# Kernel optimization log

Hardware: AMD Instinct MI355X
Metric: run time of the kernel (lower is better)

The kernel has to match this reference:

```python
import jax, jax.numpy as jnp
import numpy as np

N, E = 100000, 1000000
IN_C, OUT_C, EDGE_D = 64, 16, 8


def setup_inputs() -> dict:
    key = jax.random.key(0)
    ks = jax.random.split(key, 11)
    s = 0.1  # param scale
    return {
        "x": jax.random.normal(ks[0], (N, IN_C), jnp.float32),
        "edge_attr": jax.random.normal(ks[1], (E, EDGE_D), jnp.float32),
        "col": jax.random.randint(ks[2], (E,), 0, N, jnp.int32),
        "W_lin": jax.random.normal(ks[3], (IN_C, OUT_C), jnp.float32) * s,
        "b_lin": jax.random.normal(ks[4], (OUT_C,), jnp.float32) * s,
        "W_edge": jax.random.normal(ks[5], (EDGE_D, OUT_C), jnp.float32) * s,
        "b_edge": jax.random.normal(ks[6], (OUT_C,), jnp.float32) * s,
        "w1": jax.random.normal(ks[7], (OUT_C,), jnp.float32) * s,  # Linear(1, C) weight
        "b1": jax.random.normal(ks[8], (OUT_C,), jnp.float32) * s,
        "w2": jax.random.normal(ks[9], (OUT_C,), jnp.float32) * s,  # Linear(C, 1) weight
        "b2": jax.random.normal(ks[10], (1,), jnp.float32) * s,
    }


def reference(x, edge_attr, col, W_lin, b_lin, W_edge, b_edge, w1, b1, w2, b2):
    # node transform: [N, C]
    h = x @ W_lin + b_lin
    # edge attr transform: [E, C]
    ea = edge_attr @ W_edge + b_edge
    # gather source node features per edge: [E, C]
    nv = h[col]
    # [E, 2C]
    combined = jnp.concatenate([nv, ea], axis=-1)
    # per-scalar MLP: Linear(1,C) -> ReLU -> Linear(C,1)
    # hid: [E, 2C, C]; scores: [E, 2C]
    hid = jax.nn.relu(combined[..., None] * w1 + b1)
    scores = hid @ w2 + b2
    # softmax over the 2C axis
    attn = jax.nn.softmax(scores, axis=1)
    # repeat_interleave(2, dim=1): each feature column duplicated -> [E, 2C]
    nv2 = jnp.repeat(nv, 2, axis=1)
    return nv2 * attn
```

## Files before the change

### kernel.cpp

```cpp
#include <hip/hip_runtime.h>
#include <math.h>

#define IN_C 64
#define OUT_C 16

typedef float f4 __attribute__((ext_vector_type(4)));
typedef float f2 __attribute__((ext_vector_type(2)));

__global__ __launch_bounds__(256) void node_linear_kernel(
    const float* __restrict__ x, const float* __restrict__ W_lin,
    const float* __restrict__ b_lin, float* __restrict__ h, int N)
{
    __shared__ float sW[IN_C * OUT_C];
    __shared__ float sb[OUT_C];
    for (int i = threadIdx.x; i < IN_C * OUT_C; i += blockDim.x) sW[i] = W_lin[i];
    if (threadIdx.x < OUT_C) sb[threadIdx.x] = b_lin[threadIdx.x];
    __syncthreads();

    int n = blockIdx.x * blockDim.x + threadIdx.x;
    if (n >= N) return;

    float acc[OUT_C];
    #pragma unroll
    for (int j = 0; j < OUT_C; j++) acc[j] = sb[j];

    const f4* xr = (const f4*)(x + (size_t)n * IN_C);
    #pragma unroll
    for (int k4 = 0; k4 < IN_C / 4; k4++) {
        f4 xv = __builtin_nontemporal_load(xr + k4);
        #pragma unroll
        for (int kk = 0; kk < 4; kk++) {
            const int k = k4 * 4 + kk;
            const float xs = xv[kk];
            const f4* wrow = (const f4*)(sW + k * OUT_C);
            #pragma unroll
            for (int jq = 0; jq < 4; jq++) {
                f4 wv = wrow[jq];
                acc[jq * 4 + 0] = fmaf(xs, wv[0], acc[jq * 4 + 0]);
                acc[jq * 4 + 1] = fmaf(xs, wv[1], acc[jq * 4 + 1]);
                acc[jq * 4 + 2] = fmaf(xs, wv[2], acc[jq * 4 + 2]);
                acc[jq * 4 + 3] = fmaf(xs, wv[3], acc[jq * 4 + 3]);
            }
        }
    }

    f4* hr = (f4*)(h + (size_t)n * OUT_C);
    #pragma unroll
    for (int jq = 0; jq < 4; jq++) {
        f4 o;
        o[0] = acc[jq * 4 + 0]; o[1] = acc[jq * 4 + 1];
        o[2] = acc[jq * 4 + 2]; o[3] = acc[jq * 4 + 3];
        hr[jq] = o;
    }
}

__global__ __launch_bounds__(256) void edge_attn8_kernel(
    const float* __restrict__ edge_attr, const int* __restrict__ col,
    const float* __restrict__ h,
    const float* __restrict__ W_edge, const float* __restrict__ b_edge,
    const float* __restrict__ w1, const float* __restrict__ b1,
    const float* __restrict__ w2, const float* __restrict__ b2,
    float* __restrict__ out, int E)
{
    __shared__ float sWe[8 * OUT_C];
    __shared__ float sbe[OUT_C];
    if (threadIdx.x < 32)
        ((f4*)sWe)[threadIdx.x] = ((const f4*)W_edge)[threadIdx.x];
    if (threadIdx.x >= 32 && threadIdx.x < 36)
        ((f4*)sbe)[threadIdx.x - 32] = ((const f4*)b_edge)[threadIdx.x - 32];
    __syncthreads();

    const int tid  = blockIdx.x * 256 + threadIdx.x;
    const int e    = tid >> 3;
    if (e >= E) return;
    const int lane = threadIdx.x & 63;
    const int sub  = lane & 7;

    const int c = col[e];
    const f2* hp = (const f2*)(h + (size_t)c * OUT_C);
    f2 nv2 = hp[sub];

    const f4* ep = (const f4*)(edge_attr + (size_t)e * 8);
    f4 eaA = ep[0], eaB = ep[1];
    float ear[8] = {eaA[0], eaA[1], eaA[2], eaA[3],
                    eaB[0], eaB[1], eaB[2], eaB[3]};

    float w1v[16], b1u[16], su[16];
    float P = 0.f, Qv;
    {
        float Q = b2[0];
        #pragma unroll
        for (int j = 0; j < 16; j++) {
            float a = w1[j], b = b1[j], s = 0.5f * w2[j];
            b1u[j] = b; su[j] = s;
            P = fmaf(a, s, P);
            Q = fmaf(b, s, Q);
            asm("v_mov_b32 %0, %1" : "=v"(w1v[j]) : "s"(a));
        }
        asm("v_mov_b32 %0, %1" : "=v"(Qv) : "s"(Q));
    }

    const f2* sWe2 = (const f2*)sWe;
    const f2* sbe2 = (const f2*)sbe;
    f2 bpair = sbe2[sub];
    float eax = bpair[0], eay = bpair[1];
    #pragma unroll
    for (int d = 0; d < 8; d++) {
        f2 w = sWe2[d * 8 + sub];
        eax = fmaf(ear[d], w[0], eax);
        eay = fmaf(ear[d], w[1], eay);
    }

    const int srcA = (lane & 56) | (2 * (sub & 3));
    const int srcB = srcA | 1;
    float cv[4];
    {
        float a0 = __shfl(nv2[0], srcA, 64), a1 = __shfl(nv2[1], srcA, 64);
        float a2 = __shfl(nv2[0], srcB, 64), a3 = __shfl(nv2[1], srcB, 64);
        float b0 = __shfl(eax,    srcA, 64), b1s = __shfl(eay,   srcA, 64);
        float b2s = __shfl(eax,   srcB, 64), b3 = __shfl(eay,    srcB, 64);
        const bool lo = (sub < 4);
        cv[0] = lo ? a0 : b0;   cv[1] = lo ? a1 : b1s;
        cv[2] = lo ? a2 : b2s;  cv[3] = lo ? a3 : b3;
    }

    float ex[4];
    #pragma unroll
    for (int q = 0; q < 4; q++) {
        float acc = fmaf(P, cv[q], Qv);
        #pragma unroll
        for (int j = 0; j < 16; j++) {
            float t = fmaf(cv[q], w1v[j], b1u[j]);
            acc = fmaf(fabsf(t), su[j], acc);
        }
        ex[q] = __expf(acc);
    }

    float psum = (ex[0] + ex[1]) + (ex[2] + ex[3]);
    psum += __shfl_xor(psum, 1, 64);
    psum += __shfl_xor(psum, 2, 64);
    psum += __shfl_xor(psum, 4, 64);
    const float inv = __builtin_amdgcn_rcpf(psum);

    f4 o;
    o[0] = nv2[0] * ex[0] * inv;
    o[1] = nv2[0] * ex[1] * inv;
    o[2] = nv2[1] * ex[2] * inv;
    o[3] = nv2[1] * ex[3] * inv;
    ((f4*)(out + (size_t)e * 32))[sub] = o;
}

extern "C" void kernel_launch(void* const* d_in, const int* in_sizes, int n_in,
                              void* d_out, int out_size, void* d_ws, size_t ws_size,
                              hipStream_t stream) {
    const float* x         = (const float*)d_in[0];
    const float* edge_attr = (const float*)d_in[1];
    const int*   col       = (const int*)d_in[2];
    const float* W_lin     = (const float*)d_in[3];
    const float* b_lin     = (const float*)d_in[4];
    const float* W_edge    = (const float*)d_in[5];
    const float* b_edge    = (const float*)d_in[6];
    const float* w1        = (const float*)d_in[7];
    const float* b1        = (const float*)d_in[8];
    const float* w2        = (const float*)d_in[9];
    const float* b2        = (const float*)d_in[10];
    float* out = (float*)d_out;

    const int N = in_sizes[0] / IN_C;
    const int E = in_sizes[1] / 8;

    float* h = (float*)d_ws;

    dim3 blk(256);
    dim3 grid1((N + 255) / 256);
    node_linear_kernel<<<grid1, blk, 0, stream>>>(x, W_lin, b_lin, h, N);

    long long total = (long long)E * 8;
    dim3 grid2((unsigned)((total + 255) / 256));
    edge_attn8_kernel<<<grid2, blk, 0, stream>>>(edge_attr, col, h,
                                                 W_edge, b_edge, w1, b1, w2, b2,
                                                 out, E);
}
```

Measured before the change: 79.65 us.

## Precompute per-node softmax exponentials in node kernel, edge kernel scores edge features only

The node-side half of the per-scalar MLP scores depends only on the node, so the node kernel now computes those 16 exponentials and their sum once per node and stores them in workspace. The edge kernel gathers them by `col` and only evaluates the 16 edge-attribute scores, roughly halving its MLP arithmetic. The ReLU MLP is folded into |c + b/w|·|w|·s/2 terms held in a small constants buffer filled by an extra setup kernel. The cost is more workspace traffic (exn and sumN writes plus extra gathers), one more launch, and a division by w1 that assumes no zero weights.

```diff
diff --git a/kernel.cpp b/kernel.cpp
--- a/kernel.cpp
+++ b/kernel.cpp
@@ -7,9 +7,35 @@
 typedef float f4 __attribute__((ext_vector_type(4)));
 typedef float f2 __attribute__((ext_vector_type(2)));
 
+
+__global__ void setup_cst_kernel(const float* __restrict__ w1,
+                                 const float* __restrict__ b1,
+                                 const float* __restrict__ w2,
+                                 const float* __restrict__ b2,
+                                 float* __restrict__ cst)
+{
+    int j = threadIdx.x;
+    if (j < 16) {
+        float w = w1[j], b = b1[j], s = 0.5f * w2[j];
+        cst[2 + j]  = b / w;
+        cst[18 + j] = s * fabsf(w);
+    }
+    if (j == 0) {
+        float P = 0.f, Q = b2[0];
+        for (int k = 0; k < 16; k++) {
+            float s = 0.5f * w2[k];
+            P = fmaf(w1[k], s, P);
+            Q = fmaf(b1[k], s, Q);
+        }
+        cst[0] = P; cst[1] = Q;
+    }
+}
+
 __global__ __launch_bounds__(256) void node_linear_kernel(
     const float* __restrict__ x, const float* __restrict__ W_lin,
-    const float* __restrict__ b_lin, float* __restrict__ h, int N)
+    const float* __restrict__ b_lin, const float* __restrict__ cst,
+    float* __restrict__ h, float* __restrict__ exn, float* __restrict__ sumN,
+    int N)
 {
     __shared__ float sW[IN_C * OUT_C];
     __shared__ float sb[OUT_C];
@@ -30,9 +56,8 @@
         f4 xv = __builtin_nontemporal_load(xr + k4);
         #pragma unroll
         for (int kk = 0; kk < 4; kk++) {
-            const int k = k4 * 4 + kk;
             const float xs = xv[kk];
-            const f4* wrow = (const f4*)(sW + k * OUT_C);
+            const f4* wrow = (const f4*)(sW + (k4 * 4 + kk) * OUT_C);
             #pragma unroll
             for (int jq = 0; jq < 4; jq++) {
                 f4 wv = wrow[jq];
@@ -44,22 +69,39 @@
         }
     }
 
+    const float P = cst[0], Q = cst[1];
+    float ex[OUT_C];
+    float sum = 0.f;
+    #pragma unroll
+    for (int k = 0; k < OUT_C; k++) {
+        const float cv = acc[k];
+        float a = fmaf(P, cv, Q);
+        #pragma unroll
+        for (int j = 0; j < 16; j++)
+            a = fmaf(fabsf(cv + cst[2 + j]), cst[18 + j], a);
+        float e = __expf(a);
+        ex[k] = e;
+        sum += e;
+    }
+
     f4* hr = (f4*)(h + (size_t)n * OUT_C);
+    f4* xr2 = (f4*)(exn + (size_t)n * OUT_C);
     #pragma unroll
     for (int jq = 0; jq < 4; jq++) {
-        f4 o;
-        o[0] = acc[jq * 4 + 0]; o[1] = acc[jq * 4 + 1];
-        o[2] = acc[jq * 4 + 2]; o[3] = acc[jq * 4 + 3];
+        f4 o, p;
+        o[0] = acc[jq*4+0]; o[1] = acc[jq*4+1]; o[2] = acc[jq*4+2]; o[3] = acc[jq*4+3];
+        p[0] = ex[jq*4+0];  p[1] = ex[jq*4+1];  p[2] = ex[jq*4+2];  p[3] = ex[jq*4+3];
         hr[jq] = o;
-    }
+        xr2[jq] = p;
+    }
+    sumN[n] = sum;
 }
 
 __global__ __launch_bounds__(256) void edge_attn8_kernel(
     const float* __restrict__ edge_attr, const int* __restrict__ col,
-    const float* __restrict__ h,
     const float* __restrict__ W_edge, const float* __restrict__ b_edge,
-    const float* __restrict__ w1, const float* __restrict__ b1,
-    const float* __restrict__ w2, const float* __restrict__ b2,
+    const float* __restrict__ cst, const float* __restrict__ h,
+    const float* __restrict__ exn, const float* __restrict__ sumN,
     float* __restrict__ out, int E)
 {
     __shared__ float sWe[8 * OUT_C];
@@ -70,84 +112,70 @@
         ((f4*)sbe)[threadIdx.x - 32] = ((const f4*)b_edge)[threadIdx.x - 32];
     __syncthreads();
 
-    const int tid  = blockIdx.x * 256 + threadIdx.x;
-    const int e    = tid >> 3;
-    if (e >= E) return;
+    const int tid = blockIdx.x * 256 + threadIdx.x;
+    int e = tid >> 3;
+    const bool valid = e < E;
+    if (!valid) e = E - 1;
     const int lane = threadIdx.x & 63;
     const int sub  = lane & 7;
 
     const int c = col[e];
-    const f2* hp = (const f2*)(h + (size_t)c * OUT_C);
-    f2 nv2 = hp[sub];
+    f2 nv2 = ((const f2*)(h   + (size_t)c * OUT_C))[sub];
+    f2 xn2 = ((const f2*)(exn + (size_t)c * OUT_C))[sub];
+    const float sN = sumN[c];
 
     const f4* ep = (const f4*)(edge_attr + (size_t)e * 8);
     f4 eaA = ep[0], eaB = ep[1];
     float ear[8] = {eaA[0], eaA[1], eaA[2], eaA[3],
                     eaB[0], eaB[1], eaB[2], eaB[3]};
 
-    float w1v[16], b1u[16], su[16];
-    float P = 0.f, Qv;
-    {
-        float Q = b2[0];
-        #pragma unroll
-        for (int j = 0; j < 16; j++) {
-            float a = w1[j], b = b1[j], s = 0.5f * w2[j];
-            b1u[j] = b; su[j] = s;
-            P = fmaf(a, s, P);
-            Q = fmaf(b, s, Q);
-            asm("v_mov_b32 %0, %1" : "=v"(w1v[j]) : "s"(a));
-        }
-        asm("v_mov_b32 %0, %1" : "=v"(Qv) : "s"(Q));
-    }
-
-    const f2* sWe2 = (const f2*)sWe;
-    const f2* sbe2 = (const f2*)sbe;
-    f2 bpair = sbe2[sub];
-    float eax = bpair[0], eay = bpair[1];
+    f2 bp = ((const f2*)sbe)[sub];
+    float eax = bp[0], eay = bp[1];
     #pragma unroll
     for (int d = 0; d < 8; d++) {
-        f2 w = sWe2[d * 8 + sub];
+        f2 w = ((const f2*)sWe)[d * 8 + sub];
         eax = fmaf(ear[d], w[0], eax);
         eay = fmaf(ear[d], w[1], eay);
     }
 
-    const int srcA = (lane & 56) | (2 * (sub & 3));
-    const int srcB = srcA | 1;
-    float cv[4];
-    {
-        float a0 = __shfl(nv2[0], srcA, 64), a1 = __shfl(nv2[1], srcA, 64);
-        float a2 = __shfl(nv2[0], srcB, 64), a3 = __shfl(nv2[1], srcB, 64);
-        float b0 = __shfl(eax,    srcA, 64), b1s = __shfl(eay,   srcA, 64);
-        float b2s = __shfl(eax,   srcB, 64), b3 = __shfl(eay,    srcB, 64);
-        const bool lo = (sub < 4);
-        cv[0] = lo ? a0 : b0;   cv[1] = lo ? a1 : b1s;
-        cv[2] = lo ? a2 : b2s;  cv[3] = lo ? a3 : b3;
-    }
-
-    float ex[4];
-    #pragma unroll
-    for (int q = 0; q < 4; q++) {
-        float acc = fmaf(P, cv[q], Qv);
-        #pragma unroll
-        for (int j = 0; j < 16; j++) {
-            float t = fmaf(cv[q], w1v[j], b1u[j]);
-            acc = fmaf(fabsf(t), su[j], acc);
-        }
-        ex[q] = __expf(acc);
-    }
-
-    float psum = (ex[0] + ex[1]) + (ex[2] + ex[3]);
-    psum += __shfl_xor(psum, 1, 64);
-    psum += __shfl_xor(psum, 2, 64);
-    psum += __shfl_xor(psum, 4, 64);
-    const float inv = __builtin_amdgcn_rcpf(psum);
-
-    f4 o;
-    o[0] = nv2[0] * ex[0] * inv;
-    o[1] = nv2[0] * ex[1] * inv;
-    o[2] = nv2[1] * ex[2] * inv;
-    o[3] = nv2[1] * ex[3] * inv;
-    ((f4*)(out + (size_t)e * 32))[sub] = o;
+    const float P = cst[0], Q = cst[1];
+    float a0 = fmaf(P, eax, Q);
+    float a1 = fmaf(P, eay, Q);
+    #pragma unroll
+    for (int j = 0; j < 16; j++) {
+        const float r  = cst[2 + j];
+        const float sp = cst[18 + j];
+        a0 = fmaf(fabsf(eax + r), sp, a0);
+        a1 = fmaf(fabsf(eay + r), sp, a1);
+    }
+    const float ex0 = __expf(a0);
+    const float ex1 = __expf(a1);
+
+    float ps = ex0 + ex1;
+    ps += __shfl_xor(ps, 1, 64);
+    ps += __shfl_xor(ps, 2, 64);
+    ps += __shfl_xor(ps, 4, 64);
+    const float inv = __builtin_amdgcn_rcpf(sN + ps);
+
+    const int srcA = (lane & 56) | (sub >> 1);
+    const int srcB = srcA | 4;
+    float a0v = __shfl(nv2[0], srcA, 64);
+    float a1v = __shfl(nv2[1], srcA, 64);
+    float b0v = __shfl(nv2[0], srcB, 64);
+    float b1v = __shfl(nv2[1], srcB, 64);
+    const bool odd = (sub & 1);
+    const float nvA = odd ? a1v : a0v;
+    const float nvB = odd ? b1v : b0v;
+
+    if (valid) {
+        const float sA = nvA * inv, sB = nvB * inv;
+        f2 o01, o23;
+        o01[0] = sA * xn2[0];  o01[1] = sA * xn2[1];
+        o23[0] = sB * ex0;     o23[1] = sB * ex1;
+        f2* op = (f2*)(out + (size_t)e * 32);
+        op[sub]     = o01;
+        op[8 + sub] = o23;
+    }
 }
 
 extern "C" void kernel_launch(void* const* d_in, const int* in_sizes, int n_in,
@@ -169,15 +197,20 @@
     const int N = in_sizes[0] / IN_C;
     const int E = in_sizes[1] / 8;
 
-    float* h = (float*)d_ws;
+    float* cst  = (float*)d_ws;
+    float* h    = cst + 64;
+    float* exn  = h + (size_t)N * OUT_C;
+    float* sumN = exn + (size_t)N * OUT_C;
+
+    setup_cst_kernel<<<1, 64, 0, stream>>>(w1, b1, w2, b2, cst);
 
     dim3 blk(256);
     dim3 grid1((N + 255) / 256);
-    node_linear_kernel<<<grid1, blk, 0, stream>>>(x, W_lin, b_lin, h, N);
+    node_linear_kernel<<<grid1, blk, 0, stream>>>(x, W_lin, b_lin, cst,
+                                                  h, exn, sumN, N);
 
     long long total = (long long)E * 8;
     dim3 grid2((unsigned)((total + 255) / 256));
-    edge_attn8_kernel<<<grid2, blk, 0, stream>>>(edge_attr, col, h,
-                                                 W_edge, b_edge, w1, b1, w2, b2,
-                                                 out, E);
-}
+    edge_attn8_kernel<<<grid2, blk, 0, stream>>>(edge_attr, col, W_edge, b_edge,
+                                                 cst, h, exn, sumN, out, E);
+}
```

New measurement: 94.58 us. 18.7% more time.
